# Performance work log

Measured on AMD Instinct MI355X. Metric: run time of the kernel, lower is better.

Reference implementation:

```python
import jax, jax.numpy as jnp
import numpy as np

ROWS, COLS, NFEAT = 128, 128, 256
BATCH = 4096


def setup_inputs() -> dict:
    key = jax.random.key(0)
    k1, k2 = jax.random.split(key)
    xb = jax.random.normal(k1, (BATCH, NFEAT), dtype=jnp.float32)
    weights = jax.random.normal(k2, (ROWS, COLS, NFEAT), dtype=jnp.float32)
    return {"xb": xb, "weights": weights}


def reference(xb, weights):
    # Flatten codebook: (M, F) with M = rows*cols
    w = weights.reshape(-1, NFEAT)
    # Pairwise Euclidean distances via ||a||^2 + ||b||^2 - 2 a.b (single GEMM)
    a2 = jnp.sum(xb * xb, axis=-1, keepdims=True)            # (B, 1)
    b2 = jnp.sum(w * w, axis=-1)                             # (M,)
    d2 = a2 + b2[None, :] - 2.0 * jnp.einsum('bf,mf->bm', xb, w)  # (B, M)
    distances = jnp.sqrt(jnp.maximum(d2, 0.0))
    # BMU: argmin over codebook, converted to 2D map indices
    min_idxs = jnp.argmin(distances, axis=-1)                # (B,)
    bmus = jnp.stack([min_idxs // COLS, min_idxs % COLS], axis=-1)  # (B, 2)
    return bmus
```

## Files before the change

### kernel.cpp

```cpp
#include <hip/hip_runtime.h>
#include <cfloat>

#define NFEAT 256
#define BATCH 4096
#define MTOT  16384
#define NSTRIP 32
#define STRIPW 512
#define NCH 32
#define UMARGIN 0.75f

typedef __attribute__((ext_vector_type(8))) short bf16x8;
typedef __attribute__((ext_vector_type(4))) float f32x4;

#define GP(p)   ((const __attribute__((address_space(1))) void*)(p))
#define LDSP(p) ((__attribute__((address_space(3))) void*)(p))

__device__ __forceinline__ unsigned bf16pack(float a, float b) {
    unsigned ua = __float_as_uint(a), ub = __float_as_uint(b);
    unsigned ra = (ua + 0x7fffu + ((ua >> 16) & 1u)) >> 16;
    unsigned rb = (ub + 0x7fffu + ((ub >> 16) & 1u)) >> 16;
    return ra | (rb << 16);
}

__global__ __launch_bounds__(256) void prep_a_kernel(const float* __restrict__ xb,
                                                     uint2* __restrict__ Abf,
                                                     float* __restrict__ a2) {
    int gid  = blockIdx.x * blockDim.x + threadIdx.x;
    int row  = gid >> 6;
    int lane = gid & 63;
    float4 v = ((const float4*)(xb + (size_t)row * NFEAT))[lane];
    Abf[(size_t)row * 64 + lane] = make_uint2(bf16pack(v.x, v.y), bf16pack(v.z, v.w));
    float s = v.x * v.x + v.y * v.y + v.z * v.z + v.w * v.w;
    #pragma unroll
    for (int off = 32; off > 0; off >>= 1) s += __shfl_down(s, off);
    if (lane == 0) a2[row] = s;
}

__global__ __launch_bounds__(256) void prep_b_kernel(const float* __restrict__ w,
                                                     uint4* __restrict__ Bfr,
                                                     float* __restrict__ b2) {
    const int t = threadIdx.x, l = t & 63;
    const int g = blockIdx.x * 4 + (t >> 6);
    const int col = g * 16 + (l & 15);
    const float4* src = (const float4*)w;
    float ss = 0.f;
    #pragma unroll
    for (int kk = 0; kk < 8; ++kk) {
        float4 v0 = src[(size_t)col * 64 + kk * 8 + (l >> 4) * 2];
        float4 v1 = src[(size_t)col * 64 + kk * 8 + (l >> 4) * 2 + 1];
        ss += v0.x * v0.x + v0.y * v0.y + v0.z * v0.z + v0.w * v0.w
            + v1.x * v1.x + v1.y * v1.y + v1.z * v1.z + v1.w * v1.w;
        uint4 o;
        o.x = bf16pack(v0.x, v0.y);
        o.y = bf16pack(v0.z, v0.w);
        o.z = bf16pack(v1.x, v1.y);
        o.w = bf16pack(v1.z, v1.w);
        Bfr[(size_t)g * 512 + kk * 64 + l] = o;
    }
    ss += __shfl_xor(ss, 16);
    ss += __shfl_xor(ss, 32);
    if (l < 16) b2[g * 16 + l] = ss;
}

__global__ __launch_bounds__(512, 2) void som_mfma_kernel(
        const unsigned short* __restrict__ Abf, const unsigned short* __restrict__ Bfr,
        const float* __restrict__ b2, float* __restrict__ part) {
    __shared__ char smem[67584];

    const int t = threadIdx.x, l = t & 63;
    const int wid = t >> 6;
    const int x = blockIdx.x & 7, y = blockIdx.x >> 3;
    const int strip = x * 4 + (y & 3);
    const int m0 = (y >> 2) * 512 + wid * 64;

    const char* gA = (const char*)Abf + (size_t)(m0 + (l & 15)) * 512 + (l >> 4) * 16;
    bf16x8 afr[4][8];
    #pragma unroll
    for (int m = 0; m < 4; ++m)
        #pragma unroll
        for (int kk = 0; kk < 8; ++kk)
            afr[m][kk] = *(const bf16x8*)(gA + m * 8192 + kk * 64);
    #pragma unroll
    for (int m = 0; m < 4; ++m)
        #pragma unroll
        for (int kk = 0; kk < 8; ++kk)
            asm volatile("" : "+v"(afr[m][kk]));

    const char* gBs = (const char*)Bfr + (size_t)strip * 262144 + t * 16;

    __builtin_amdgcn_global_load_lds(GP((const char*)b2 + (size_t)strip * 2048 + t * 4),
                                     LDSP(smem + 65536 + t * 4), 4, 0, 0);
    #pragma unroll
    for (int c = 0; c < 4; ++c)
        __builtin_amdgcn_global_load_lds(GP(gBs + c * 8192),
                                         LDSP(smem + c * 8192 + t * 16), 16, 0, 0);

    float r0[4][4], r1[4][4];
    #pragma unroll
    for (int m = 0; m < 4; ++m)
        #pragma unroll
        for (int j = 0; j < 4; ++j) { r0[m][j] = -FLT_MAX; r1[m][j] = -FLT_MAX; }

    for (int c = 0; c < NCH; ++c) {
        if (c < NCH - 4) asm volatile("s_waitcnt vmcnt(3)" ::: "memory");
        else             asm volatile("s_waitcnt vmcnt(0)" ::: "memory");
        __builtin_amdgcn_s_barrier();
        asm volatile("" ::: "memory");

        if (c + 4 < NCH)
            __builtin_amdgcn_global_load_lds(GP(gBs + (size_t)(c + 4) * 8192),
                LDSP(smem + ((c + 4) & 7) * 8192 + t * 16), 16, 0, 0);

        const float b2c = *(const float*)(smem + 65536 + (c * 16 + (l & 15)) * 4);
        const float bi = -0.5f * b2c;
        f32x4 acc[4];
        #pragma unroll
        for (int m = 0; m < 4; ++m) acc[m] = (f32x4){bi, bi, bi, bi};

        const char* buf = smem + (c & 7) * 8192;
        __builtin_amdgcn_s_setprio(1);
        #pragma unroll
        for (int kk = 0; kk < 8; ++kk) {
            bf16x8 bf = *(const bf16x8*)(buf + kk * 1024 + l * 16);
            #pragma unroll
            for (int m = 0; m < 4; ++m)
                acc[m] = __builtin_amdgcn_mfma_f32_16x16x32_bf16(afr[m][kk], bf,
                                                                 acc[m], 0, 0, 0);
        }
        __builtin_amdgcn_s_setprio(0);

        const unsigned idn = (unsigned)c;
        #pragma unroll
        for (int m = 0; m < 4; ++m)
            #pragma unroll
            for (int j = 0; j < 4; ++j) {
                float p = __uint_as_float((__float_as_uint(acc[m][j]) & 0xFFFFFFE0u) | idn);
                float nr1 = __builtin_amdgcn_fmed3f(r0[m][j], r1[m][j], p);
                r0[m][j] = fmaxf(r0[m][j], p);
                r1[m][j] = nr1;
            }
    }

    #pragma unroll
    for (int m = 0; m < 4; ++m)
        #pragma unroll
        for (int j = 0; j < 4; ++j) {
            unsigned u0 = __float_as_uint(r0[m][j]);
            unsigned u1 = __float_as_uint(r1[m][j]);
            u0 = (u0 & 0xFFFFFE00u) | ((u0 & 31u) << 4) | (unsigned)(l & 15);
            u1 = (u1 & 0xFFFFFE00u) | ((u1 & 31u) << 4) | (unsigned)(l & 15);
            float v0 = __uint_as_float(u0), v1 = __uint_as_float(u1);
            #pragma unroll
            for (int off = 1; off < 16; off <<= 1) {
                float o0 = __shfl_xor(v0, off), o1 = __shfl_xor(v1, off);
                float nv1 = fmaxf(fminf(v0, o0), fmaxf(v1, o1));
                v0 = fmaxf(v0, o0);
                v1 = nv1;
            }
            if ((l & 15) == 0) {
                int row = m0 + m * 16 + (l >> 4) * 4 + j;
                ((float2*)part)[(size_t)row * NSTRIP + strip] = make_float2(v0, v1);
            }
        }
}

__global__ __launch_bounds__(256) void refine_kernel(
        const float* __restrict__ xb, const float* __restrict__ w,
        const float* __restrict__ a2, const float* __restrict__ b2,
        const float* __restrict__ part, int* __restrict__ out) {
    const int t = threadIdx.x, l = t & 63;
    const int row = blockIdx.x * 4 + (t >> 6);

    const float v = part[(size_t)row * (NSTRIP * 2) + l];
    float mx = v;
    #pragma unroll
    for (int off = 1; off < 64; off <<= 1) mx = fmaxf(mx, __shfl_xor(mx, off));
    const float cut = mx - UMARGIN;

    unsigned long long key = ~0ull;
    if (v >= cut) {
        unsigned b = __float_as_uint(v);
        int lane4 = b & 15, ch = (b >> 4) & 31, strip = l >> 1;
        int col = strip * STRIPW + ch * 16 + lane4;
        const float4* xr = (const float4*)(xb + (size_t)row * NFEAT);
        const float4* wr = (const float4*)(w + (size_t)col * NFEAT);
        float s0 = 0.f, s1 = 0.f, s2 = 0.f, s3 = 0.f;
        #pragma unroll
        for (int k = 0; k < 16; ++k) {
            float4 x0 = xr[4 * k + 0], w0 = wr[4 * k + 0];
            float4 x1 = xr[4 * k + 1], w1 = wr[4 * k + 1];
            float4 x2 = xr[4 * k + 2], w2 = wr[4 * k + 2];
            float4 x3 = xr[4 * k + 3], w3 = wr[4 * k + 3];
            s0 += x0.x * w0.x + x0.y * w0.y + x0.z * w0.z + x0.w * w0.w;
            s1 += x1.x * w1.x + x1.y * w1.y + x1.z * w1.z + x1.w * w1.w;
            s2 += x2.x * w2.x + x2.y * w2.y + x2.z * w2.z + x2.w * w2.w;
            s3 += x3.x * w3.x + x3.y * w3.y + x3.z * w3.z + x3.w * w3.w;
        }
        float dot = (s0 + s1) + (s2 + s3);
        float dd = a2[row] + b2[col] - 2.f * dot;
        float s = sqrtf(fmaxf(dd, 0.f));
        key = ((unsigned long long)__float_as_uint(s) << 32) | (unsigned)col;
    }
    #pragma unroll
    for (int off = 1; off < 64; off <<= 1) {
        unsigned long long o = __shfl_xor(key, off);
        key = o < key ? o : key;
    }
    if (l == 0) {
        int idx = (int)(key & 0xffffffffu);
        out[2 * row]     = idx >> 7;
        out[2 * row + 1] = idx & 127;
    }
}

extern "C" void kernel_launch(void* const* d_in, const int* in_sizes, int n_in,
                              void* d_out, int out_size, void* d_ws, size_t ws_size,
                              hipStream_t stream) {
    const float* xb = (const float*)d_in[0];
    const float* w  = (const float*)d_in[1];
    int* out = (int*)d_out;

    char* ws = (char*)d_ws;
    unsigned short* Abf = (unsigned short*)ws;
    unsigned short* Bfr = (unsigned short*)(ws + (2u << 20));
    float* a2   = (float*)(ws + (10u << 20));
    float* b2   = (float*)(ws + (10u << 20) + (64u << 10));
    float* part = (float*)(ws + (10u << 20) + (128u << 10));

    prep_a_kernel<<<(BATCH * 64) / 256, 256, 0, stream>>>(xb, (uint2*)Abf, a2);
    prep_b_kernel<<<MTOT / 64, 256, 0, stream>>>(w, (uint4*)Bfr, b2);
    som_mfma_kernel<<<256, 512, 0, stream>>>(Abf, Bfr, b2, part);
    refine_kernel<<<BATCH / 4, 256, 0, stream>>>(xb, w, a2, b2, part, out);
}
```

Measured before the change: 77.26 us.

## Switch distance GEMM to 32x32 MFMA tiles, fuse prep kernels

Replaces the 16x16x32 bf16 MFMA tiling with 32x32x16 MFMAs. The GEMM is reorganized into 256-thread blocks (512 blocks) with 16 KB B chunks, a 4-slot LDS ring and a 3-deep prefetch. The two preprocessing kernels are merged into one launch, and B is repacked into the 32-wide fragment layout. The per-chunk index encoding in the packed candidate keys and in refine is adjusted to the new 16-chunk x 32-column layout. This aims to cut MFMA issue count and launch overhead, but it changes occupancy and register pressure.

```diff
diff --git a/kernel.cpp b/kernel.cpp
--- a/kernel.cpp
+++ b/kernel.cpp
@@ -6,11 +6,11 @@
 #define MTOT  16384
 #define NSTRIP 32
 #define STRIPW 512
-#define NCH 32
+#define NCH 16
 #define UMARGIN 0.75f
 
 typedef __attribute__((ext_vector_type(8))) short bf16x8;
-typedef __attribute__((ext_vector_type(4))) float f32x4;
+typedef __attribute__((ext_vector_type(16))) float f32x16;
 
 #define GP(p)   ((const __attribute__((address_space(1))) void*)(p))
 #define LDSP(p) ((__attribute__((address_space(3))) void*)(p))
@@ -22,47 +22,43 @@
     return ra | (rb << 16);
 }
 
-__global__ __launch_bounds__(256) void prep_a_kernel(const float* __restrict__ xb,
-                                                     uint2* __restrict__ Abf,
-                                                     float* __restrict__ a2) {
-    int gid  = blockIdx.x * blockDim.x + threadIdx.x;
-    int row  = gid >> 6;
-    int lane = gid & 63;
-    float4 v = ((const float4*)(xb + (size_t)row * NFEAT))[lane];
-    Abf[(size_t)row * 64 + lane] = make_uint2(bf16pack(v.x, v.y), bf16pack(v.z, v.w));
-    float s = v.x * v.x + v.y * v.y + v.z * v.z + v.w * v.w;
-    #pragma unroll
-    for (int off = 32; off > 0; off >>= 1) s += __shfl_down(s, off);
-    if (lane == 0) a2[row] = s;
-}
-
-__global__ __launch_bounds__(256) void prep_b_kernel(const float* __restrict__ w,
-                                                     uint4* __restrict__ Bfr,
-                                                     float* __restrict__ b2) {
+__global__ __launch_bounds__(256) void prep_kernel(
+        const float* __restrict__ xb, const float* __restrict__ w,
+        uint2* __restrict__ Abf, uint4* __restrict__ Bfr,
+        float* __restrict__ a2, float* __restrict__ b2) {
     const int t = threadIdx.x, l = t & 63;
-    const int g = blockIdx.x * 4 + (t >> 6);
-    const int col = g * 16 + (l & 15);
-    const float4* src = (const float4*)w;
-    float ss = 0.f;
-    #pragma unroll
-    for (int kk = 0; kk < 8; ++kk) {
-        float4 v0 = src[(size_t)col * 64 + kk * 8 + (l >> 4) * 2];
-        float4 v1 = src[(size_t)col * 64 + kk * 8 + (l >> 4) * 2 + 1];
-        ss += v0.x * v0.x + v0.y * v0.y + v0.z * v0.z + v0.w * v0.w
-            + v1.x * v1.x + v1.y * v1.y + v1.z * v1.z + v1.w * v1.w;
-        uint4 o;
-        o.x = bf16pack(v0.x, v0.y);
-        o.y = bf16pack(v0.z, v0.w);
-        o.z = bf16pack(v1.x, v1.y);
-        o.w = bf16pack(v1.z, v1.w);
-        Bfr[(size_t)g * 512 + kk * 64 + l] = o;
-    }
-    ss += __shfl_xor(ss, 16);
-    ss += __shfl_xor(ss, 32);
-    if (l < 16) b2[g * 16 + l] = ss;
-}
-
-__global__ __launch_bounds__(512, 2) void som_mfma_kernel(
+    const int wv = blockIdx.x * 4 + (t >> 6);
+    if (wv < BATCH) {
+        float4 v = ((const float4*)(xb + (size_t)wv * NFEAT))[l];
+        Abf[(size_t)wv * 64 + l] = make_uint2(bf16pack(v.x, v.y), bf16pack(v.z, v.w));
+        float s = v.x * v.x + v.y * v.y + v.z * v.z + v.w * v.w;
+        #pragma unroll
+        for (int off = 32; off > 0; off >>= 1) s += __shfl_down(s, off);
+        if (l == 0) a2[wv] = s;
+    } else {
+        const int g = wv - BATCH;
+        const int col = g * 32 + (l & 31);
+        const float4* src = (const float4*)(w + (size_t)col * NFEAT);
+        float ss = 0.f;
+        #pragma unroll
+        for (int ks = 0; ks < 16; ++ks) {
+            float4 v0 = src[ks * 4 + (l >> 5) * 2];
+            float4 v1 = src[ks * 4 + (l >> 5) * 2 + 1];
+            ss += v0.x * v0.x + v0.y * v0.y + v0.z * v0.z + v0.w * v0.w
+                + v1.x * v1.x + v1.y * v1.y + v1.z * v1.z + v1.w * v1.w;
+            uint4 o;
+            o.x = bf16pack(v0.x, v0.y);
+            o.y = bf16pack(v0.z, v0.w);
+            o.z = bf16pack(v1.x, v1.y);
+            o.w = bf16pack(v1.z, v1.w);
+            Bfr[(size_t)g * 1024 + ks * 64 + l] = o;
+        }
+        ss += __shfl_xor(ss, 32);
+        if (l < 32) b2[g * 32 + l] = ss;
+    }
+}
+
+__global__ __launch_bounds__(256, 2) void som_mfma_kernel(
         const unsigned short* __restrict__ Abf, const unsigned short* __restrict__ Bfr,
         const float* __restrict__ b2, float* __restrict__ part) {
     __shared__ char smem[67584];
@@ -71,97 +67,105 @@
     const int wid = t >> 6;
     const int x = blockIdx.x & 7, y = blockIdx.x >> 3;
     const int strip = x * 4 + (y & 3);
-    const int m0 = (y >> 2) * 512 + wid * 64;
-
-    const char* gA = (const char*)Abf + (size_t)(m0 + (l & 15)) * 512 + (l >> 4) * 16;
-    bf16x8 afr[4][8];
-    #pragma unroll
-    for (int m = 0; m < 4; ++m)
-        #pragma unroll
-        for (int kk = 0; kk < 8; ++kk)
-            afr[m][kk] = *(const bf16x8*)(gA + m * 8192 + kk * 64);
-    #pragma unroll
-    for (int m = 0; m < 4; ++m)
-        #pragma unroll
-        for (int kk = 0; kk < 8; ++kk)
-            asm volatile("" : "+v"(afr[m][kk]));
-
-    const char* gBs = (const char*)Bfr + (size_t)strip * 262144 + t * 16;
-
-    __builtin_amdgcn_global_load_lds(GP((const char*)b2 + (size_t)strip * 2048 + t * 4),
-                                     LDSP(smem + 65536 + t * 4), 4, 0, 0);
-    #pragma unroll
-    for (int c = 0; c < 4; ++c)
-        __builtin_amdgcn_global_load_lds(GP(gBs + c * 8192),
-                                         LDSP(smem + c * 8192 + t * 16), 16, 0, 0);
-
-    float r0[4][4], r1[4][4];
-    #pragma unroll
-    for (int m = 0; m < 4; ++m)
-        #pragma unroll
-        for (int j = 0; j < 4; ++j) { r0[m][j] = -FLT_MAX; r1[m][j] = -FLT_MAX; }
+    const int m0 = (y >> 2) * 256 + wid * 64;
+
+    const char* gA = (const char*)Abf + (size_t)(m0 + (l & 31)) * 512 + (l >> 5) * 16;
+    bf16x8 afr[2][16];
+    #pragma unroll
+    for (int mt = 0; mt < 2; ++mt)
+        #pragma unroll
+        for (int ks = 0; ks < 16; ++ks)
+            afr[mt][ks] = *(const bf16x8*)(gA + mt * 32 * 512 + ks * 32);
+
+    const char* gBs = (const char*)Bfr + (size_t)strip * (NCH * 16384) + t * 16;
+#define STAGE(slot, c) {                                                         \
+        _Pragma("unroll")                                                        \
+        for (int i_ = 0; i_ < 4; ++i_)                                           \
+            __builtin_amdgcn_global_load_lds(                                    \
+                GP(gBs + (size_t)(c) * 16384 + i_ * 4096),                       \
+                LDSP(smem + (slot) * 16384 + i_ * 4096 + t * 16), 16, 0, 0);     \
+    }
+
+    #pragma unroll
+    for (int j = 0; j < 2; ++j)
+        __builtin_amdgcn_global_load_lds(
+            GP((const char*)b2 + (size_t)strip * 2048 + j * 1024 + t * 4),
+            LDSP(smem + 65536 + j * 1024 + t * 4), 4, 0, 0);
+    STAGE(0, 0) STAGE(1, 1) STAGE(2, 2)
+
+    #pragma unroll
+    for (int mt = 0; mt < 2; ++mt)
+        #pragma unroll
+        for (int ks = 0; ks < 16; ++ks)
+            asm volatile("" : "+v"(afr[mt][ks]));
+
+    float r0[2][16], r1[2][16];
+    #pragma unroll
+    for (int mt = 0; mt < 2; ++mt)
+        #pragma unroll
+        for (int r = 0; r < 16; ++r) { r0[mt][r] = -FLT_MAX; r1[mt][r] = -FLT_MAX; }
 
     for (int c = 0; c < NCH; ++c) {
-        if (c < NCH - 4) asm volatile("s_waitcnt vmcnt(3)" ::: "memory");
-        else             asm volatile("s_waitcnt vmcnt(0)" ::: "memory");
+        if      (c < 14) asm volatile("s_waitcnt vmcnt(8)" ::: "memory");
+        else if (c == 14) asm volatile("s_waitcnt vmcnt(4)" ::: "memory");
+        else              asm volatile("s_waitcnt vmcnt(0)" ::: "memory");
         __builtin_amdgcn_s_barrier();
         asm volatile("" ::: "memory");
 
-        if (c + 4 < NCH)
-            __builtin_amdgcn_global_load_lds(GP(gBs + (size_t)(c + 4) * 8192),
-                LDSP(smem + ((c + 4) & 7) * 8192 + t * 16), 16, 0, 0);
-
-        const float b2c = *(const float*)(smem + 65536 + (c * 16 + (l & 15)) * 4);
+        if (c + 3 < NCH) STAGE((c + 3) & 3, c + 3)
+
+        const float b2c = *(const float*)(smem + 65536 + (c * 32 + (l & 31)) * 4);
         const float bi = -0.5f * b2c;
-        f32x4 acc[4];
-        #pragma unroll
-        for (int m = 0; m < 4; ++m) acc[m] = (f32x4){bi, bi, bi, bi};
-
-        const char* buf = smem + (c & 7) * 8192;
+        f32x16 acc0, acc1;
+        #pragma unroll
+        for (int r = 0; r < 16; ++r) { acc0[r] = bi; acc1[r] = bi; }
+
+        const char* buf = smem + (c & 3) * 16384;
         __builtin_amdgcn_s_setprio(1);
         #pragma unroll
-        for (int kk = 0; kk < 8; ++kk) {
-            bf16x8 bf = *(const bf16x8*)(buf + kk * 1024 + l * 16);
-            #pragma unroll
-            for (int m = 0; m < 4; ++m)
-                acc[m] = __builtin_amdgcn_mfma_f32_16x16x32_bf16(afr[m][kk], bf,
-                                                                 acc[m], 0, 0, 0);
+        for (int ks = 0; ks < 16; ++ks) {
+            bf16x8 bf = *(const bf16x8*)(buf + ks * 1024 + l * 16);
+            acc0 = __builtin_amdgcn_mfma_f32_32x32x16_bf16(afr[0][ks], bf, acc0, 0, 0, 0);
+            acc1 = __builtin_amdgcn_mfma_f32_32x32x16_bf16(afr[1][ks], bf, acc1, 0, 0, 0);
         }
         __builtin_amdgcn_s_setprio(0);
 
         const unsigned idn = (unsigned)c;
         #pragma unroll
-        for (int m = 0; m < 4; ++m)
-            #pragma unroll
-            for (int j = 0; j < 4; ++j) {
-                float p = __uint_as_float((__float_as_uint(acc[m][j]) & 0xFFFFFFE0u) | idn);
-                float nr1 = __builtin_amdgcn_fmed3f(r0[m][j], r1[m][j], p);
-                r0[m][j] = fmaxf(r0[m][j], p);
-                r1[m][j] = nr1;
-            }
-    }
-
-    #pragma unroll
-    for (int m = 0; m < 4; ++m)
-        #pragma unroll
-        for (int j = 0; j < 4; ++j) {
-            unsigned u0 = __float_as_uint(r0[m][j]);
-            unsigned u1 = __float_as_uint(r1[m][j]);
-            u0 = (u0 & 0xFFFFFE00u) | ((u0 & 31u) << 4) | (unsigned)(l & 15);
-            u1 = (u1 & 0xFFFFFE00u) | ((u1 & 31u) << 4) | (unsigned)(l & 15);
+        for (int r = 0; r < 16; ++r) {
+            float pa = __uint_as_float((__float_as_uint(acc0[r]) & 0xFFFFFFF0u) | idn);
+            float na = __builtin_amdgcn_fmed3f(r0[0][r], r1[0][r], pa);
+            r0[0][r] = fmaxf(r0[0][r], pa);
+            r1[0][r] = na;
+            float pb = __uint_as_float((__float_as_uint(acc1[r]) & 0xFFFFFFF0u) | idn);
+            float nb = __builtin_amdgcn_fmed3f(r0[1][r], r1[1][r], pb);
+            r0[1][r] = fmaxf(r0[1][r], pb);
+            r1[1][r] = nb;
+        }
+    }
+
+    #pragma unroll
+    for (int mt = 0; mt < 2; ++mt)
+        #pragma unroll
+        for (int r = 0; r < 16; ++r) {
+            unsigned u0 = __float_as_uint(r0[mt][r]);
+            unsigned u1 = __float_as_uint(r1[mt][r]);
+            u0 = (u0 & 0xFFFFFE00u) | ((u0 & 15u) << 5) | (unsigned)(l & 31);
+            u1 = (u1 & 0xFFFFFE00u) | ((u1 & 15u) << 5) | (unsigned)(l & 31);
             float v0 = __uint_as_float(u0), v1 = __uint_as_float(u1);
             #pragma unroll
-            for (int off = 1; off < 16; off <<= 1) {
+            for (int off = 1; off < 32; off <<= 1) {
                 float o0 = __shfl_xor(v0, off), o1 = __shfl_xor(v1, off);
                 float nv1 = fmaxf(fminf(v0, o0), fmaxf(v1, o1));
                 v0 = fmaxf(v0, o0);
                 v1 = nv1;
             }
-            if ((l & 15) == 0) {
-                int row = m0 + m * 16 + (l >> 4) * 4 + j;
+            if ((l & 31) == 0) {
+                int row = m0 + mt * 32 + (r & 3) + 8 * (r >> 2) + 4 * (l >> 5);
                 ((float2*)part)[(size_t)row * NSTRIP + strip] = make_float2(v0, v1);
             }
         }
+#undef STAGE
 }
 
 __global__ __launch_bounds__(256) void refine_kernel(
@@ -180,8 +184,8 @@
     unsigned long long key = ~0ull;
     if (v >= cut) {
         unsigned b = __float_as_uint(v);
-        int lane4 = b & 15, ch = (b >> 4) & 31, strip = l >> 1;
-        int col = strip * STRIPW + ch * 16 + lane4;
+        int c5 = b & 31, c4 = (b >> 5) & 15, strip = l >> 1;
+        int col = strip * STRIPW + c4 * 32 + c5;
         const float4* xr = (const float4*)(xb + (size_t)row * NFEAT);
         const float4* wr = (const float4*)(w + (size_t)col * NFEAT);
         float s0 = 0.f, s1 = 0.f, s2 = 0.f, s3 = 0.f;
@@ -227,8 +231,8 @@
     float* b2   = (float*)(ws + (10u << 20) + (64u << 10));
     float* part = (float*)(ws + (10u << 20) + (128u << 10));
 
-    prep_a_kernel<<<(BATCH * 64) / 256, 256, 0, stream>>>(xb, (uint2*)Abf, a2);
-    prep_b_kernel<<<MTOT / 64, 256, 0, stream>>>(w, (uint4*)Bfr, b2);
-    som_mfma_kernel<<<256, 512, 0, stream>>>(Abf, Bfr, b2, part);
+    prep_kernel<<<(BATCH + 512) / 4, 256, 0, stream>>>(xb, w, (uint2*)Abf,
+                                                       (uint4*)Bfr, a2, b2);
+    som_mfma_kernel<<<512, 256, 0, stream>>>(Abf, Bfr, b2, part);
     refine_kernel<<<BATCH / 4, 256, 0, stream>>>(xb, w, a2, b2, part, out);
 }
```

Result: slower. 83.67 us (+8.3%).
